# Kernel optimization log

Hardware: AMD Instinct MI355X
Metric: run time of the kernel (lower is better)

Reference implementation:

```python
import jax, jax.numpy as jnp
import numpy as np

IOU_POS = 0.6
IOU_NEG = 0.45
BOX_W, CLS_W, INT_W = 1.0, 1.0, 0.5
ALPHA, GAMMA = 0.25, 2.0
BETA = 1.0 / 9.0
EPS = 1e-6


def setup_inputs() -> dict:
    key = jax.random.key(0)
    ks = jax.random.split(key, 8)
    B, N, M, C = 8, 131072, 48, 8
    cls_logits = jax.random.normal(ks[0], (B, N, 1), jnp.float32)
    box_preds = jax.random.normal(ks[1], (B, N, 6), jnp.float32) * 0.1
    intention_logits = jax.random.normal(ks[2], (B, N, C), jnp.float32)
    # anchors: 256x256 BEV grid over 100x100m, 2 orientations -> 131072 anchors
    side = int(np.sqrt(N // 2))
    xs = jnp.linspace(0.0, 100.0, side)
    gx, gy = jnp.meshgrid(xs, xs, indexing='ij')
    base = jnp.stack([gx.ravel(), gy.ravel()], axis=-1)  # [side^2, 2]
    n0 = side * side
    a0 = jnp.concatenate([base, jnp.full((n0, 1), 2.0), jnp.full((n0, 1), 4.5), jnp.zeros((n0, 1))], axis=-1)
    a1 = a0.at[:, 4].set(jnp.pi / 2)
    anchors = jnp.concatenate([a0, a1], axis=0)  # [N, 5] xywha
    gt_xy = jax.random.uniform(ks[3], (B, M, 2), minval=0.0, maxval=100.0)
    gt_w = jax.random.uniform(ks[4], (B, M, 1), minval=1.8, maxval=2.6)
    gt_l = jax.random.uniform(ks[5], (B, M, 1), minval=4.0, maxval=5.5)
    gt_a = jax.random.uniform(ks[6], (B, M, 1), minval=-jnp.pi, maxval=jnp.pi)
    gt_boxes = jnp.concatenate([gt_xy, gt_w, gt_l, gt_a], axis=-1)  # [B, M, 5]
    gt_intentions = jax.random.randint(ks[7], (B, M), 0, C, dtype=jnp.int32)
    return dict(cls_logits=cls_logits, box_preds=box_preds, intention_logits=intention_logits,
                anchors=anchors, gt_boxes=gt_boxes, gt_intentions=gt_intentions)


def _aa_iou(anchors, gt):
    # axis-aligned IoU on center-format boxes; anchors [N,5], gt [M,5] -> [N,M]
    ah = anchors[:, 2:4] * 0.5
    gh = gt[:, 2:4] * 0.5
    amin = anchors[:, None, :2] - ah[:, None]
    amax = anchors[:, None, :2] + ah[:, None]
    gmin = gt[None, :, :2] - gh[None]
    gmax = gt[None, :, :2] + gh[None]
    wh = jnp.clip(jnp.minimum(amax, gmax) - jnp.maximum(amin, gmin), 0.0)
    inter = wh[..., 0] * wh[..., 1]
    area_a = anchors[:, 2] * anchors[:, 3]
    area_g = gt[:, 2] * gt[:, 3]
    return inter / (area_a[:, None] + area_g[None, :] - inter + EPS)


def _assign(anchors, gt_b, gt_i):
    # single-sample target assignment; anchors [N,5], gt_b [M,5], gt_i [M]
    N = anchors.shape[0]
    M = gt_b.shape[0]
    iou = _aa_iou(anchors, gt_b)                       # [N, M]
    max_iou = iou.max(axis=1)                          # [N]
    argmax_gt = iou.argmax(axis=1)                     # [N]
    neg = max_iou < IOU_NEG
    pos = max_iou >= IOU_POS
    # force-match: best anchor per GT becomes positive if its IoU >= neg thresh
    force_idx = iou.argmax(axis=0)                     # [M]
    force_iou = iou[force_idx, jnp.arange(M)]          # [M]
    forced = jnp.zeros((N,), jnp.int32).at[force_idx].add((force_iou >= IOU_NEG).astype(jnp.int32)) > 0
    pos = pos | forced
    cls_t = jnp.where(pos, 1, jnp.where(neg, 0, -1))   # [N] in {-1,0,1}
    # box delta encode against the per-anchor best GT
    ag = gt_b[argmax_gt]                               # [N, 5]
    dx = (ag[:, 0] - anchors[:, 0]) / (anchors[:, 2] + EPS)
    dy = (ag[:, 1] - anchors[:, 1]) / (anchors[:, 3] + EPS)
    dw = jnp.log(ag[:, 2] / (anchors[:, 2] + EPS) + EPS)
    dl = jnp.log(ag[:, 3] / (anchors[:, 3] + EPS) + EPS)
    da = ag[:, 4] - anchors[:, 4]
    deltas = jnp.stack([dx, dy, dw, dl, jnp.sin(da), jnp.cos(da)], axis=1)  # [N,6]
    box_t = jnp.where(pos[:, None], deltas, 0.0)
    int_t = jnp.where(pos, gt_i[argmax_gt], -1)
    return cls_t, box_t, int_t


def reference(cls_logits, box_preds, intention_logits, anchors, gt_boxes, gt_intentions):
    cls_t, box_t, int_t = jax.vmap(_assign, in_axes=(None, 0, 0))(anchors, gt_boxes, gt_intentions)
    cls_t = cls_t.reshape(-1)
    box_t = box_t.reshape(-1, 6)
    int_t = int_t.reshape(-1)
    x = cls_logits.reshape(-1)
    bp = box_preds.reshape(-1, 6)
    il = intention_logits.reshape(-1, intention_logits.shape[-1])
    valid = cls_t >= 0
    pos = cls_t == 1
    num_pos = pos.sum()
    denom = jnp.maximum(1, num_pos).astype(jnp.float32)
    # sigmoid focal loss (sum over valid) / num_pos
    t = (cls_t == 1).astype(jnp.float32)
    ce = jnp.maximum(x, 0.0) - x * t + jnp.log1p(jnp.exp(-jnp.abs(x)))
    p = jax.nn.sigmoid(x)
    p_t = p * t + (1.0 - p) * (1.0 - t)
    alpha_t = ALPHA * t + (1.0 - ALPHA) * (1.0 - t)
    focal = alpha_t * ce * (1.0 - p_t) ** GAMMA
    cls_loss = jnp.where(valid, focal, 0.0).sum() / denom
    # smooth L1 (sum over positives) / num_pos
    d = jnp.abs(bp - box_t)
    sl1 = jnp.where(d < BETA, 0.5 * d * d / BETA, d - 0.5 * BETA)
    box_loss = jnp.where(pos[:, None], sl1, 0.0).sum() / denom
    # cross-entropy over positives / num_pos (no weights, no downsampling)
    logp = jax.nn.log_softmax(il, axis=-1)
    tgt = jnp.clip(int_t, 0, il.shape[-1] - 1)
    nll = -jnp.take_along_axis(logp, tgt[:, None], axis=1)[:, 0]
    intent_loss = jnp.where(pos, nll, 0.0).sum() / denom
    total = CLS_W * cls_loss + BOX_W * box_loss + INT_W * intent_loss
    return total, cls_loss, box_loss, intent_loss, num_pos.astype(jnp.float32)
```

## Files before the change

kernel.cpp:

```cpp
#include <hip/hip_runtime.h>
#include <cstddef>

#define IOU_POS_T 0.6f
#define IOU_NEG_T 0.45f
#define F_EPS 1e-6f
#define F_ALPHA 0.25f
#define F_BETA (1.0f/9.0f)
#define MAXM 64
#define PPB 512
#define BINF 3.402823466e+38f

__device__ __forceinline__ void fp_barrier(float& x) { asm volatile("" : "+v"(x)); }
__device__ __forceinline__ unsigned long long ullmax(unsigned long long a, unsigned long long b) {
    return a > b ? a : b;
}

__global__ void __launch_bounds__(256)
dl_assign(const float* __restrict__ anchors, const float* __restrict__ gt_boxes,
          unsigned long long* __restrict__ cells, unsigned long long* __restrict__ masks,
          int N, int M, int B, int nrole0, int nblkx)
{
    const int tid = threadIdx.x;
    if ((int)blockIdx.x >= nrole0) {
        const int bblk = blockIdx.x - nrole0;
        const int pbase = bblk * PPB;
        float bmnx = BINF, bmny = BINF, bmxx = -BINF, bmxy = -BINF;
        #pragma unroll
        for (int k = 0; k < 2; ++k) {
            const int p = pbase + k * 256 + tid;
            const float* a = anchors + (size_t)p * 5;
            float ax = a[0], ay = a[1], aw = a[2], al = a[3];
            bmnx = fminf(bmnx, ax - aw * 0.5f); bmny = fminf(bmny, ay - al * 0.5f);
            bmxx = fmaxf(bmxx, ax + aw * 0.5f); bmxy = fmaxf(bmxy, ay + al * 0.5f);
        }
        #pragma unroll
        for (int off = 32; off; off >>= 1) {
            bmnx = fminf(bmnx, __shfl_xor(bmnx, off));
            bmny = fminf(bmny, __shfl_xor(bmny, off));
            bmxx = fmaxf(bmxx, __shfl_xor(bmxx, off));
            bmxy = fmaxf(bmxy, __shfl_xor(bmxy, off));
        }
        __shared__ float wbb[4][4];
        const int wave = tid >> 6;
        if ((tid & 63) == 0) { wbb[wave][0] = bmnx; wbb[wave][1] = bmny; wbb[wave][2] = bmxx; wbb[wave][3] = bmxy; }
        __syncthreads();
        if (tid < 64) {
            float cmnx = fminf(fminf(wbb[0][0], wbb[1][0]), fminf(wbb[2][0], wbb[3][0]));
            float cmny = fminf(fminf(wbb[0][1], wbb[1][1]), fminf(wbb[2][1], wbb[3][1]));
            float cmxx = fmaxf(fmaxf(wbb[0][2], wbb[1][2]), fmaxf(wbb[2][2], wbb[3][2]));
            float cmxy = fmaxf(fmaxf(wbb[0][3], wbb[1][3]), fmaxf(wbb[2][3], wbb[3][3]));
            for (int b = 0; b < B; ++b) {
                bool ov = false;
                if (tid < M) {
                    const float* g = gt_boxes + ((size_t)b * M + tid) * 5;
                    float cx = g[0], cy = g[1], hw = g[2] * 0.5f, hl = g[3] * 0.5f;
                    float wxb = fminf(cmxx, cx + hw) - fmaxf(cmnx, cx - hw);
                    float wyb = fminf(cmxy, cy + hl) - fmaxf(cmny, cy - hl);
                    ov = (wxb > 0.0f) && (wyb > 0.0f);
                }
                unsigned long long bal = __ballot(ov);
                if (tid == 0) masks[(size_t)b * nblkx + bblk] = bal;
            }
        }
        return;
    }

    const int p = blockIdx.x;
    const float* g = gt_boxes + (size_t)p * 5;
    const float cx = g[0], cy = g[1], gw_ = g[2], gl_ = g[3];
    const float hw = gw_ * 0.5f, hl = gl_ * 0.5f;
    const float gmnx = cx - hw, gmny = cy - hl, gmxx = cx + hw, gmxy = cy + hl;
    const float garea = gw_ * gl_;

    const int side = (int)sqrtf((float)(N / 2) + 0.5f);
    const float step = 100.0f / (float)(side - 1);
    const float hwx = (gw_ + 2.0f) * 0.5f;
    const float hwy = (gl_ + 4.5f) * 0.5f;
    int gx0 = (int)floorf((cx - hwx) / step) - 2; gx0 = gx0 < 0 ? 0 : gx0;
    int gx1 = (int)ceilf ((cx + hwx) / step) + 2; gx1 = gx1 > side-1 ? side-1 : gx1;
    int gy0 = (int)floorf((cy - hwy) / step) - 2; gy0 = gy0 < 0 ? 0 : gy0;
    int gy1 = (int)ceilf ((cy + hwy) / step) + 2; gy1 = gy1 > side-1 ? side-1 : gy1;
    const int nyw = gy1 - gy0 + 1;
    const int cnt = (gx1 - gx0 + 1) * nyw;

    unsigned long long best = 0ull;
    for (int idx = tid; idx < cnt; idx += 256) {
        const int col = idx / nyw, row = idx - col * nyw;
        const int i = (gx0 + col) * side + (gy0 + row);
        const float* a = anchors + (size_t)i * 5;
        float ax = a[0], ay = a[1], aw = a[2], al = a[3];
        float amnx = ax - aw * 0.5f, amny = ay - al * 0.5f;
        float amxx = ax + aw * 0.5f, amxy = ay + al * 0.5f;
        float area_a = aw * al; fp_barrier(area_a);
        float wx = fminf(amxx, gmxx) - fmaxf(amnx, gmnx); wx = fmaxf(wx, 0.0f);
        float wy = fminf(amxy, gmxy) - fmaxf(amny, gmny); wy = fmaxf(wy, 0.0f);
        float inter = wx * wy; fp_barrier(inter);
        if (inter > 0.0f) {
            float denom = (area_a + garea) - inter + F_EPS;
            float iou = inter / denom;
            unsigned long long key =
                ((unsigned long long)__float_as_uint(iou) << 32) | (unsigned)(~(unsigned)i);
            best = ullmax(best, key);
        }
    }
    #pragma unroll
    for (int off = 32; off; off >>= 1)
        best = ullmax(best, (unsigned long long)__shfl_down(best, off));
    __shared__ unsigned long long wred[4];
    if ((tid & 63) == 0) wred[tid >> 6] = best;
    __syncthreads();
    if (tid == 0)
        cells[p] = ullmax(ullmax(wred[0], wred[1]), ullmax(wred[2], wred[3]));
}

__global__ void __launch_bounds__(256, 8)
dl_loss(const float* __restrict__ cls_logits, const float* __restrict__ box_preds,
        const float* __restrict__ intent_logits, const float* __restrict__ anchors,
        const float* __restrict__ gt_boxes, const int* __restrict__ gt_ints,
        const unsigned long long* __restrict__ cells,
        const unsigned long long* __restrict__ masks,
        float4* __restrict__ parts, int N, int M, int C, int nblkx)
{
    const int b = blockIdx.y;
    const int tid = threadIdx.x;
    const int blk = blockIdx.x;
    const int pbase = blk * PPB;
    const int half = N >> 1;
    const int wave = tid >> 6;
    const unsigned long long sm = masks[(size_t)b * nblkx + blk];

    __shared__ float q0[4], q1[4], q2[4], q3[4];

    float x0[2], x1[2];
    #pragma unroll
    for (int k = 0; k < 2; ++k) {
        const int p = pbase + k * 256 + tid;
        x0[k] = cls_logits[(size_t)b * N + p];
        x1[k] = cls_logits[(size_t)b * N + half + p];
    }

    float cls_acc = 0.0f, box_acc = 0.0f, int_acc = 0.0f, np_acc = 0.0f;

    if (sm == 0ull) {
        #pragma unroll
        for (int k = 0; k < 2; ++k) {
            {
                float x = x0[k];
                float ce = fmaxf(x, 0.0f) + log1pf(expf(-fabsf(x)));
                float pp = 1.0f / (1.0f + expf(-x));
                cls_acc += (1.0f - F_ALPHA) * ce * (pp * pp);
            }
            {
                float x = x1[k];
                float ce = fmaxf(x, 0.0f) + log1pf(expf(-fabsf(x)));
                float pp = 1.0f / (1.0f + expf(-x));
                cls_acc += (1.0f - F_ALPHA) * ce * (pp * pp);
            }
        }
    } else {
        __shared__ float gmnx[MAXM], gmny[MAXM], gmxx[MAXM], gmxy[MAXM], gar[MAXM];
        __shared__ float gcx[MAXM], gcy[MAXM], gw[MAXM], gl[MAXM], ga[MAXM];
        __shared__ int gint[MAXM];
        __shared__ unsigned char sforce[PPB];

        sforce[tid] = 0; sforce[tid + 256] = 0;
        if (tid < M) {
            const float* g = gt_boxes + ((size_t)b * M + tid) * 5;
            float cx = g[0], cy = g[1], w_ = g[2], l_ = g[3], ang = g[4];
            float hw = w_ * 0.5f, hl = l_ * 0.5f;
            gmnx[tid] = cx - hw; gmny[tid] = cy - hl;
            gmxx[tid] = cx + hw; gmxy[tid] = cy + hl;
            gar[tid]  = w_ * l_;
            gcx[tid] = cx; gcy[tid] = cy; gw[tid] = w_; gl[tid] = l_; ga[tid] = ang;
            gint[tid] = gt_ints[(size_t)b * M + tid];
        }
        float ax[2], ay[2], aw[2], al[2], aah0[2], aah1[2];
        #pragma unroll
        for (int k = 0; k < 2; ++k) {
            const int p = pbase + k * 256 + tid;
            const float* a = anchors + (size_t)p * 5;
            ax[k] = a[0]; ay[k] = a[1]; aw[k] = a[2]; al[k] = a[3]; aah0[k] = a[4];
            aah1[k] = anchors[(size_t)(p + half) * 5 + 4];
        }
        __syncthreads();
        if (tid < M) {
            unsigned long long cell = cells[(size_t)b * M + tid];
            float fiou = __uint_as_float((unsigned)(cell >> 32));
            int fi = (int)(~(unsigned)cell);
            if (fiou >= IOU_NEG_T && fi >= pbase && fi < pbase + PPB) sforce[fi - pbase] = 1;
        }
        __syncthreads();

        #pragma unroll
        for (int k = 0; k < 2; ++k) {
            const int p = pbase + k * 256 + tid;
            const float amnx = ax[k] - aw[k] * 0.5f, amny = ay[k] - al[k] * 0.5f;
            const float amxx = ax[k] + aw[k] * 0.5f, amxy = ay[k] + al[k] * 0.5f;
            float area_a = aw[k] * al[k]; fp_barrier(area_a);
            unsigned long long mask = sm;
            float bestv = 0.0f; int bestm = 0;
            while (mask) {
                const int m = (int)__builtin_ctzll(mask); mask &= mask - 1;
                float wx = fminf(amxx, gmxx[m]) - fmaxf(amnx, gmnx[m]); wx = fmaxf(wx, 0.0f);
                float wy = fminf(amxy, gmxy[m]) - fmaxf(amny, gmny[m]); wy = fmaxf(wy, 0.0f);
                float inter = wx * wy; fp_barrier(inter);
                if (inter > 0.0f) {
                    float denom = (area_a + gar[m]) - inter + F_EPS;
                    float iou = inter / denom;
                    if (iou > bestv) { bestv = iou; bestm = m; }
                }
            }
            const bool neg = bestv < IOU_NEG_T;
            const bool forced = sforce[k * 256 + tid] != 0;
            const bool pos0 = (bestv >= IOU_POS_T) || forced;
            const bool pos1 = (bestv >= IOU_POS_T);
            const int m = bestm;

            float dx = 0, dy = 0, dwv = 0, dlv = 0;
            if (pos0 | pos1) {
                dx = (gcx[m] - ax[k]) / (aw[k] + F_EPS);
                dy = (gcy[m] - ay[k]) / (al[k] + F_EPS);
                dwv = logf(gw[m] / (aw[k] + F_EPS) + F_EPS);
                dlv = logf(gl[m] / (al[k] + F_EPS) + F_EPS);
            }
            if (pos0 || neg) {
                float x = x0[k];
                float t = pos0 ? 1.0f : 0.0f;
                float ce = fmaxf(x, 0.0f) - x * t + log1pf(expf(-fabsf(x)));
                float pp = 1.0f / (1.0f + expf(-x));
                float p_t = pp * t + (1.0f - pp) * (1.0f - t);
                float a_t = F_ALPHA * t + (1.0f - F_ALPHA) * (1.0f - t);
                float om = 1.0f - p_t;
                cls_acc += a_t * ce * (om * om);
            }
            if (pos0) {
                np_acc += 1.0f;
                float da = ga[m] - aah0[k];
                float tgt6[6] = { dx, dy, dwv, dlv, sinf(da), cosf(da) };
                const float* bp = box_preds + ((size_t)b * N + p) * 6;
                #pragma unroll
                for (int q = 0; q < 6; ++q) {
                    float d = fabsf(bp[q] - tgt6[q]);
                    box_acc += (d < F_BETA) ? (0.5f * d * d / F_BETA) : (d - 0.5f * F_BETA);
                }
                const float* il = intent_logits + ((size_t)b * N + p) * C;
                float mx = il[0];
                for (int c = 1; c < C; ++c) mx = fmaxf(mx, il[c]);
                float se = 0.0f;
                for (int c = 0; c < C; ++c) se += expf(il[c] - mx);
                int tg = gint[m]; tg = tg < 0 ? 0 : (tg > C - 1 ? C - 1 : tg);
                int_acc += (mx + logf(se)) - il[tg];
            }
            if (pos1 || neg) {
                float x = x1[k];
                float t = pos1 ? 1.0f : 0.0f;
                float ce = fmaxf(x, 0.0f) - x * t + log1pf(expf(-fabsf(x)));
                float pp = 1.0f / (1.0f + expf(-x));
                float p_t = pp * t + (1.0f - pp) * (1.0f - t);
                float a_t = F_ALPHA * t + (1.0f - F_ALPHA) * (1.0f - t);
                float om = 1.0f - p_t;
                cls_acc += a_t * ce * (om * om);
            }
            if (pos1) {
                np_acc += 1.0f;
                const int i1 = p + half;
                float da = ga[m] - aah1[k];
                float tgt6[6] = { dx, dy, dwv, dlv, sinf(da), cosf(da) };
                const float* bp = box_preds + ((size_t)b * N + i1) * 6;
                #pragma unroll
                for (int q = 0; q < 6; ++q) {
                    float d = fabsf(bp[q] - tgt6[q]);
                    box_acc += (d < F_BETA) ? (0.5f * d * d / F_BETA) : (d - 0.5f * F_BETA);
                }
                const float* il = intent_logits + ((size_t)b * N + i1) * C;
                float mx = il[0];
                for (int c = 1; c < C; ++c) mx = fmaxf(mx, il[c]);
                float se = 0.0f;
                for (int c = 0; c < C; ++c) se += expf(il[c] - mx);
                int tg = gint[m]; tg = tg < 0 ? 0 : (tg > C - 1 ? C - 1 : tg);
                int_acc += (mx + logf(se)) - il[tg];
            }
        }
    }

    #pragma unroll
    for (int off = 32; off; off >>= 1) {
        cls_acc += __shfl_down(cls_acc, off);
        box_acc += __shfl_down(box_acc, off);
        int_acc += __shfl_down(int_acc, off);
        np_acc  += __shfl_down(np_acc, off);
    }
    if ((tid & 63) == 0) { q0[wave] = cls_acc; q1[wave] = box_acc; q2[wave] = int_acc; q3[wave] = np_acc; }
    __syncthreads();
    if (tid == 0) {
        parts[(size_t)b * nblkx + blk] =
            make_float4(q0[0] + q0[1] + q0[2] + q0[3],
                        q1[0] + q1[1] + q1[2] + q1[3],
                        q2[0] + q2[1] + q2[2] + q2[3],
                        q3[0] + q3[1] + q3[2] + q3[3]);
    }
}

__global__ void __launch_bounds__(256)
dl_reduce(const float4* __restrict__ parts, int total, float* __restrict__ out)
{
    const int tid = threadIdx.x;
    float c = 0, bx = 0, it = 0, np = 0;
    for (int k = tid; k < total; k += 256) {
        float4 v = parts[k];
        c += v.x; bx += v.y; it += v.z; np += v.w;
    }
    #pragma unroll
    for (int off = 32; off; off >>= 1) {
        c  += __shfl_down(c, off);
        bx += __shfl_down(bx, off);
        it += __shfl_down(it, off);
        np += __shfl_down(np, off);
    }
    __shared__ float q0[4], q1[4], q2[4], q3[4];
    const int wave = tid >> 6;
    if ((tid & 63) == 0) { q0[wave] = c; q1[wave] = bx; q2[wave] = it; q3[wave] = np; }
    __syncthreads();
    if (tid == 0) {
        float cs = q0[0] + q0[1] + q0[2] + q0[3];
        float bs = q1[0] + q1[1] + q1[2] + q1[3];
        float is = q2[0] + q2[1] + q2[2] + q2[3];
        float ns = q3[0] + q3[1] + q3[2] + q3[3];
        float denom = fmaxf(1.0f, ns);
        float cls = cs / denom, bo = bs / denom, in_ = is / denom;
        out[0] = cls + bo + 0.5f * in_;
        out[1] = cls;
        out[2] = bo;
        out[3] = in_;
        out[4] = ns;
    }
}

extern "C" void kernel_launch(void* const* d_in, const int* in_sizes, int n_in,
                              void* d_out, int out_size, void* d_ws, size_t ws_size,
                              hipStream_t stream) {
    const float* cls_logits    = (const float*)d_in[0];
    const float* box_preds     = (const float*)d_in[1];
    const float* intent_logits = (const float*)d_in[2];
    const float* anchors       = (const float*)d_in[3];
    const float* gt_boxes      = (const float*)d_in[4];
    const int*   gt_ints       = (const int*)d_in[5];

    const int N = in_sizes[3] / 5;
    const int B = in_sizes[0] / N;
    const int M = in_sizes[5] / B;
    const int C = in_sizes[2] / in_sizes[0];
    const int half = N / 2;
    const int nblkx = (half + PPB - 1) / PPB;
    const int nrole0 = B * M;

    char* ws = (char*)d_ws;
    unsigned long long* cells = (unsigned long long*)ws;
    size_t off = ((size_t)B * M * 8 + 255) & ~(size_t)255;
    unsigned long long* masks = (unsigned long long*)(ws + off);
    off = (off + (size_t)B * nblkx * 8 + 255) & ~(size_t)255;
    float4* parts = (float4*)(ws + off);

    dl_assign<<<nrole0 + nblkx, 256, 0, stream>>>(anchors, gt_boxes, cells, masks,
                                                  N, M, B, nrole0, nblkx);
    dim3 grid(nblkx, B);
    dl_loss<<<grid, 256, 0, stream>>>(cls_logits, box_preds, intent_logits, anchors,
                                      gt_boxes, gt_ints, cells, masks, parts, N, M, C, nblkx);
    dl_reduce<<<1, 256, 0, stream>>>(parts, nblkx * B, (float*)d_out);
}
```

Measured before the change: 31.37 us.

## Fuse assignment into loss kernel, recomputing per-GT best anchor per overlapping block

```diff
diff --git a/kernel.cpp b/kernel.cpp
--- a/kernel.cpp
+++ b/kernel.cpp
@@ -15,120 +15,26 @@
     return a > b ? a : b;
 }
 
-__global__ void __launch_bounds__(256)
-dl_assign(const float* __restrict__ anchors, const float* __restrict__ gt_boxes,
-          unsigned long long* __restrict__ cells, unsigned long long* __restrict__ masks,
-          int N, int M, int B, int nrole0, int nblkx)
-{
-    const int tid = threadIdx.x;
-    if ((int)blockIdx.x >= nrole0) {
-        const int bblk = blockIdx.x - nrole0;
-        const int pbase = bblk * PPB;
-        float bmnx = BINF, bmny = BINF, bmxx = -BINF, bmxy = -BINF;
-        #pragma unroll
-        for (int k = 0; k < 2; ++k) {
-            const int p = pbase + k * 256 + tid;
-            const float* a = anchors + (size_t)p * 5;
-            float ax = a[0], ay = a[1], aw = a[2], al = a[3];
-            bmnx = fminf(bmnx, ax - aw * 0.5f); bmny = fminf(bmny, ay - al * 0.5f);
-            bmxx = fmaxf(bmxx, ax + aw * 0.5f); bmxy = fmaxf(bmxy, ay + al * 0.5f);
-        }
-        #pragma unroll
-        for (int off = 32; off; off >>= 1) {
-            bmnx = fminf(bmnx, __shfl_xor(bmnx, off));
-            bmny = fminf(bmny, __shfl_xor(bmny, off));
-            bmxx = fmaxf(bmxx, __shfl_xor(bmxx, off));
-            bmxy = fmaxf(bmxy, __shfl_xor(bmxy, off));
-        }
-        __shared__ float wbb[4][4];
-        const int wave = tid >> 6;
-        if ((tid & 63) == 0) { wbb[wave][0] = bmnx; wbb[wave][1] = bmny; wbb[wave][2] = bmxx; wbb[wave][3] = bmxy; }
-        __syncthreads();
-        if (tid < 64) {
-            float cmnx = fminf(fminf(wbb[0][0], wbb[1][0]), fminf(wbb[2][0], wbb[3][0]));
-            float cmny = fminf(fminf(wbb[0][1], wbb[1][1]), fminf(wbb[2][1], wbb[3][1]));
-            float cmxx = fmaxf(fmaxf(wbb[0][2], wbb[1][2]), fmaxf(wbb[2][2], wbb[3][2]));
-            float cmxy = fmaxf(fmaxf(wbb[0][3], wbb[1][3]), fmaxf(wbb[2][3], wbb[3][3]));
-            for (int b = 0; b < B; ++b) {
-                bool ov = false;
-                if (tid < M) {
-                    const float* g = gt_boxes + ((size_t)b * M + tid) * 5;
-                    float cx = g[0], cy = g[1], hw = g[2] * 0.5f, hl = g[3] * 0.5f;
-                    float wxb = fminf(cmxx, cx + hw) - fmaxf(cmnx, cx - hw);
-                    float wyb = fminf(cmxy, cy + hl) - fmaxf(cmny, cy - hl);
-                    ov = (wxb > 0.0f) && (wyb > 0.0f);
-                }
-                unsigned long long bal = __ballot(ov);
-                if (tid == 0) masks[(size_t)b * nblkx + bblk] = bal;
-            }
-        }
-        return;
-    }
-
-    const int p = blockIdx.x;
-    const float* g = gt_boxes + (size_t)p * 5;
-    const float cx = g[0], cy = g[1], gw_ = g[2], gl_ = g[3];
-    const float hw = gw_ * 0.5f, hl = gl_ * 0.5f;
-    const float gmnx = cx - hw, gmny = cy - hl, gmxx = cx + hw, gmxy = cy + hl;
-    const float garea = gw_ * gl_;
-
-    const int side = (int)sqrtf((float)(N / 2) + 0.5f);
-    const float step = 100.0f / (float)(side - 1);
-    const float hwx = (gw_ + 2.0f) * 0.5f;
-    const float hwy = (gl_ + 4.5f) * 0.5f;
-    int gx0 = (int)floorf((cx - hwx) / step) - 2; gx0 = gx0 < 0 ? 0 : gx0;
-    int gx1 = (int)ceilf ((cx + hwx) / step) + 2; gx1 = gx1 > side-1 ? side-1 : gx1;
-    int gy0 = (int)floorf((cy - hwy) / step) - 2; gy0 = gy0 < 0 ? 0 : gy0;
-    int gy1 = (int)ceilf ((cy + hwy) / step) + 2; gy1 = gy1 > side-1 ? side-1 : gy1;
-    const int nyw = gy1 - gy0 + 1;
-    const int cnt = (gx1 - gx0 + 1) * nyw;
-
-    unsigned long long best = 0ull;
-    for (int idx = tid; idx < cnt; idx += 256) {
-        const int col = idx / nyw, row = idx - col * nyw;
-        const int i = (gx0 + col) * side + (gy0 + row);
-        const float* a = anchors + (size_t)i * 5;
-        float ax = a[0], ay = a[1], aw = a[2], al = a[3];
-        float amnx = ax - aw * 0.5f, amny = ay - al * 0.5f;
-        float amxx = ax + aw * 0.5f, amxy = ay + al * 0.5f;
-        float area_a = aw * al; fp_barrier(area_a);
-        float wx = fminf(amxx, gmxx) - fmaxf(amnx, gmnx); wx = fmaxf(wx, 0.0f);
-        float wy = fminf(amxy, gmxy) - fmaxf(amny, gmny); wy = fmaxf(wy, 0.0f);
-        float inter = wx * wy; fp_barrier(inter);
-        if (inter > 0.0f) {
-            float denom = (area_a + garea) - inter + F_EPS;
-            float iou = inter / denom;
-            unsigned long long key =
-                ((unsigned long long)__float_as_uint(iou) << 32) | (unsigned)(~(unsigned)i);
-            best = ullmax(best, key);
-        }
-    }
-    #pragma unroll
-    for (int off = 32; off; off >>= 1)
-        best = ullmax(best, (unsigned long long)__shfl_down(best, off));
-    __shared__ unsigned long long wred[4];
-    if ((tid & 63) == 0) wred[tid >> 6] = best;
-    __syncthreads();
-    if (tid == 0)
-        cells[p] = ullmax(ullmax(wred[0], wred[1]), ullmax(wred[2], wred[3]));
-}
-
-__global__ void __launch_bounds__(256, 8)
-dl_loss(const float* __restrict__ cls_logits, const float* __restrict__ box_preds,
-        const float* __restrict__ intent_logits, const float* __restrict__ anchors,
-        const float* __restrict__ gt_boxes, const int* __restrict__ gt_ints,
-        const unsigned long long* __restrict__ cells,
-        const unsigned long long* __restrict__ masks,
-        float4* __restrict__ parts, int N, int M, int C, int nblkx)
+__global__ void __launch_bounds__(256, 4)
+dl_fused(const float* __restrict__ cls_logits, const float* __restrict__ box_preds,
+         const float* __restrict__ intent_logits, const float* __restrict__ anchors,
+         const float* __restrict__ gt_boxes, const int* __restrict__ gt_ints,
+         float4* __restrict__ parts, int N, int M, int C, int nblkx)
 {
     const int b = blockIdx.y;
     const int tid = threadIdx.x;
     const int blk = blockIdx.x;
     const int pbase = blk * PPB;
     const int half = N >> 1;
-    const int wave = tid >> 6;
-    const unsigned long long sm = masks[(size_t)b * nblkx + blk];
-
+    const int wave = tid >> 6, lane = tid & 63;
+    const int side = (int)sqrtf((float)half + 0.5f);
+    const float step = 100.0f / (float)(side - 1);
+
+    __shared__ float gmnx[MAXM], gmny[MAXM], gmxx[MAXM], gmxy[MAXM], gar[MAXM];
+    __shared__ float gcx[MAXM], gcy[MAXM], gw[MAXM], gl[MAXM], ga[MAXM];
+    __shared__ int gint[MAXM];
+    __shared__ unsigned char sforce[PPB];
+    __shared__ unsigned long long smask_s;
     __shared__ float q0[4], q1[4], q2[4], q3[4];
 
     float x0[2], x1[2];
@@ -138,6 +44,29 @@
         x0[k] = cls_logits[(size_t)b * N + p];
         x1[k] = cls_logits[(size_t)b * N + half + p];
     }
+
+    if (tid < 64) {
+        bool ov = false;
+        if (tid < M) {
+            const float* g = gt_boxes + ((size_t)b * M + tid) * 5;
+            float cx = g[0], cy = g[1], w_ = g[2], l_ = g[3], ang = g[4];
+            float hw = w_ * 0.5f, hl = l_ * 0.5f;
+            float tmnx = cx - hw, tmxx = cx + hw;
+            gmnx[tid] = tmnx; gmny[tid] = cy - hl;
+            gmxx[tid] = tmxx; gmxy[tid] = cy + hl;
+            gar[tid]  = w_ * l_;
+            gcx[tid] = cx; gcy[tid] = cy; gw[tid] = w_; gl[tid] = l_; ga[tid] = ang;
+            gint[tid] = gt_ints[(size_t)b * M + tid];
+            float bmnx = (float)(2 * blk) * step - 1.0f - 0.01f;
+            float bmxx = (float)(2 * blk + 1) * step + 1.0f + 0.01f;
+            ov = (fminf(bmxx, tmxx) - fmaxf(bmnx, tmnx)) > 0.0f;
+        }
+        unsigned long long bal = __ballot(ov);
+        if (tid == 0) smask_s = bal;
+    }
+    sforce[tid] = 0; sforce[tid + 256] = 0;
+    __syncthreads();
+    const unsigned long long sm = smask_s;
 
     float cls_acc = 0.0f, box_acc = 0.0f, int_acc = 0.0f, np_acc = 0.0f;
 
@@ -158,21 +87,56 @@
             }
         }
     } else {
-        __shared__ float gmnx[MAXM], gmny[MAXM], gmxx[MAXM], gmxy[MAXM], gar[MAXM];
-        __shared__ float gcx[MAXM], gcy[MAXM], gw[MAXM], gl[MAXM], ga[MAXM];
-        __shared__ int gint[MAXM];
-        __shared__ unsigned char sforce[PPB];
-
-        sforce[tid] = 0; sforce[tid + 256] = 0;
-        if (tid < M) {
-            const float* g = gt_boxes + ((size_t)b * M + tid) * 5;
-            float cx = g[0], cy = g[1], w_ = g[2], l_ = g[3], ang = g[4];
-            float hw = w_ * 0.5f, hl = l_ * 0.5f;
-            gmnx[tid] = cx - hw; gmny[tid] = cy - hl;
-            gmxx[tid] = cx + hw; gmxy[tid] = cy + hl;
-            gar[tid]  = w_ * l_;
-            gcx[tid] = cx; gcy[tid] = cy; gw[tid] = w_; gl[tid] = l_; ga[tid] = ang;
-            gint[tid] = gt_ints[(size_t)b * M + tid];
+        {
+            int j = 0;
+            unsigned long long mm = sm;
+            while (mm) {
+                const int m = (int)__builtin_ctzll(mm); mm &= mm - 1;
+                if ((j & 3) == wave) {
+                    const float cxm = gcx[m], cym = gcy[m], gwm = gw[m], glm = gl[m];
+                    const float gmnxm = gmnx[m], gmnym = gmny[m];
+                    const float gmxxm = gmxx[m], gmxym = gmxy[m];
+                    const float garea = gar[m];
+                    const float hwx = (gwm + 2.0f) * 0.5f;
+                    const float hwy = (glm + 4.5f) * 0.5f;
+                    int gx0 = (int)floorf((cxm - hwx) / step) - 2; gx0 = gx0 < 0 ? 0 : gx0;
+                    int gx1 = (int)ceilf ((cxm + hwx) / step) + 2; gx1 = gx1 > side-1 ? side-1 : gx1;
+                    int gy0 = (int)floorf((cym - hwy) / step) - 2; gy0 = gy0 < 0 ? 0 : gy0;
+                    int gy1 = (int)ceilf ((cym + hwy) / step) + 2; gy1 = gy1 > side-1 ? side-1 : gy1;
+                    const int nyw = gy1 - gy0 + 1;
+                    const int cnt = (gx1 - gx0 + 1) * nyw;
+                    unsigned long long best = 0ull;
+                    for (int idx = lane; idx < cnt; idx += 64) {
+                        const int col = idx / nyw, row = idx - col * nyw;
+                        const int i = (gx0 + col) * side + (gy0 + row);
+                        const float* a = anchors + (size_t)i * 5;
+                        float ax = a[0], ay = a[1], aw = a[2], al = a[3];
+                        float amnx = ax - aw * 0.5f, amny = ay - al * 0.5f;
+                        float amxx = ax + aw * 0.5f, amxy = ay + al * 0.5f;
+                        float area_a = aw * al; fp_barrier(area_a);
+                        float wx = fminf(amxx, gmxxm) - fmaxf(amnx, gmnxm); wx = fmaxf(wx, 0.0f);
+                        float wy = fminf(amxy, gmxym) - fmaxf(amny, gmnym); wy = fmaxf(wy, 0.0f);
+                        float inter = wx * wy; fp_barrier(inter);
+                        if (inter > 0.0f) {
+                            float denom = (area_a + garea) - inter + F_EPS;
+                            float iou = inter / denom;
+                            unsigned long long key =
+                                ((unsigned long long)__float_as_uint(iou) << 32) | (unsigned)(~(unsigned)i);
+                            best = ullmax(best, key);
+                        }
+                    }
+                    #pragma unroll
+                    for (int off = 32; off; off >>= 1)
+                        best = ullmax(best, (unsigned long long)__shfl_down(best, off));
+                    if (lane == 0) {
+                        float fiou = __uint_as_float((unsigned)(best >> 32));
+                        int fi = (int)(~(unsigned)best);
+                        if (fiou >= IOU_NEG_T && fi >= pbase && fi < pbase + PPB)
+                            sforce[fi - pbase] = 1;
+                    }
+                }
+                ++j;
+            }
         }
         float ax[2], ay[2], aw[2], al[2], aah0[2], aah1[2];
         #pragma unroll
@@ -181,13 +145,6 @@
             const float* a = anchors + (size_t)p * 5;
             ax[k] = a[0]; ay[k] = a[1]; aw[k] = a[2]; al[k] = a[3]; aah0[k] = a[4];
             aah1[k] = anchors[(size_t)(p + half) * 5 + 4];
-        }
-        __syncthreads();
-        if (tid < M) {
-            unsigned long long cell = cells[(size_t)b * M + tid];
-            float fiou = __uint_as_float((unsigned)(cell >> 32));
-            int fi = (int)(~(unsigned)cell);
-            if (fiou >= IOU_NEG_T && fi >= pbase && fi < pbase + PPB) sforce[fi - pbase] = 1;
         }
         __syncthreads();
 
@@ -352,19 +309,11 @@
     const int C = in_sizes[2] / in_sizes[0];
     const int half = N / 2;
     const int nblkx = (half + PPB - 1) / PPB;
-    const int nrole0 = B * M;
-
-    char* ws = (char*)d_ws;
-    unsigned long long* cells = (unsigned long long*)ws;
-    size_t off = ((size_t)B * M * 8 + 255) & ~(size_t)255;
-    unsigned long long* masks = (unsigned long long*)(ws + off);
-    off = (off + (size_t)B * nblkx * 8 + 255) & ~(size_t)255;
-    float4* parts = (float4*)(ws + off);
-
-    dl_assign<<<nrole0 + nblkx, 256, 0, stream>>>(anchors, gt_boxes, cells, masks,
-                                                  N, M, B, nrole0, nblkx);
+
+    float4* parts = (float4*)d_ws;
+
     dim3 grid(nblkx, B);
-    dl_loss<<<grid, 256, 0, stream>>>(cls_logits, box_preds, intent_logits, anchors,
-                                      gt_boxes, gt_ints, cells, masks, parts, N, M, C, nblkx);
+    dl_fused<<<grid, 256, 0, stream>>>(cls_logits, box_preds, intent_logits, anchors,
+                                       gt_boxes, gt_ints, parts, N, M, C, nblkx);
     dl_reduce<<<1, 256, 0, stream>>>(parts, nblkx * B, (float*)d_out);
 }
```

New measurement: 32.05 us. +2.2%, slower.
